# Kernel tuning notes

Measured on AMD Instinct MI355X. Metric: run time of the kernel, lower is better.

The kernel has to match this reference:

```python
import jax, jax.numpy as jnp
import numpy as np

B, L, H, F, D = 8, 2048, 1024, 256, 3  # batch, seq, d_model, adapter bottleneck, non-news domains
EPS = 1e-6  # annotated-transformer LayerNorm eps


def setup_inputs() -> dict:
    key = jax.random.key(0)
    ks = jax.random.split(key, 6)
    s1 = 1.0 / np.sqrt(H)
    s2 = 1.0 / np.sqrt(F)
    return {
        "x": jax.random.normal(ks[0], (B, L, H), jnp.float32),
        # per-domain LayerNorm params (SublayerConnection.norm)
        "ln_g": jnp.ones((D, H), jnp.float32),
        "ln_b": jnp.zeros((D, H), jnp.float32),
        # per-domain adapter FFN: Linear(H->F), ReLU, Linear(F->H)
        "W1": (jax.random.normal(ks[1], (D, F, H), jnp.float32) * s1),
        "b1": jnp.zeros((D, F), jnp.float32),
        "W2": (jax.random.normal(ks[2], (D, H, F), jnp.float32) * s2),
        "b2": jnp.zeros((D, H), jnp.float32),
        # per-domain gate Linear(2H -> 1), split into the x-half (gu) and adapter-half (gv)
        "gu": (jax.random.normal(ks[3], (D, H), jnp.float32) * s1),
        "gv": (jax.random.normal(ks[4], (D, H), jnp.float32) * s1),
        "gb": jnp.zeros((D,), jnp.float32),
    }


def reference(x, ln_g, ln_b, W1, b1, W2, b2, gu, gv, gb):
    # mix_output=True, used_domain_list=['news','book','bible','iwslt'],
    # target_domain='book' (in list -> no extra pass), dropout=eval (identity).
    mu = jnp.mean(x, axis=-1, keepdims=True)
    sd = jnp.std(x, axis=-1, keepdims=True, ddof=1)  # torch .std default (unbiased)
    xn = (x - mu) / (sd + EPS)                        # shared normalization stats
    # per-domain LayerNorm affine -> [D,B,L,H]
    h = xn[None] * ln_g[:, None, None, :] + ln_b[:, None, None, :]
    # adapter FFN (wo_residual_forward): Linear -> ReLU -> Linear
    mid = jax.nn.relu(jnp.einsum('dblh,dfh->dblf', h, W1) + b1[:, None, None, :])
    a = jnp.einsum('dblf,dhf->dblh', mid, W2) + b2[:, None, None, :]  # [D,B,L,H]
    # gate = sigmoid(Linear([x; a])) with W_gate split as [gu | gv]
    gate = jax.nn.sigmoid(
        jnp.einsum('blh,dh->dbl', x, gu)
        + jnp.einsum('dblh,dh->dbl', a, gv)
        + gb[:, None, None]
    )  # [D,B,L]
    # stacked sum includes 'news' contribution (= x), then outer residual +x:
    return 2.0 * x + jnp.sum(gate[..., None] * a, axis=0)
```

## Files before the change

### kernel.cpp

```cpp
#include <hip/hip_runtime.h>
#include <cstdint>

#define T_TOK 16384
#define H 1024
#define F 256
#define D 3
#define DF 768

typedef unsigned short u16;
typedef __attribute__((ext_vector_type(8))) short short8;
typedef __attribute__((ext_vector_type(4))) float floatx4;

__device__ __forceinline__ u16 f2bf(float f) {
  unsigned u = __float_as_uint(f);
  u += 0x7fff + ((u >> 16) & 1);
  return (u16)(u >> 16);
}
__device__ __forceinline__ float bf2f(u16 s) {
  return __uint_as_float(((unsigned)s) << 16);
}

__device__ __forceinline__ void gload_lds16(const void* g, void* l) {
  __builtin_amdgcn_global_load_lds(
      reinterpret_cast<const __attribute__((address_space(1))) void*>(
          reinterpret_cast<uintptr_t>(g)),
      reinterpret_cast<__attribute__((address_space(3))) void*>(
          reinterpret_cast<uintptr_t>(l)),
      16, 0, 0);
}

__device__ __forceinline__ float block_reduce_256(float v, float* red, int tid) {
  #pragma unroll
  for (int o = 32; o > 0; o >>= 1) v += __shfl_xor(v, o);
  __syncthreads();
  if ((tid & 63) == 0) red[tid >> 6] = v;
  __syncthreads();
  return red[0] + red[1] + red[2] + red[3];
}


__global__ __launch_bounds__(256)
void prep_elem(const float* __restrict__ W1, const float* __restrict__ lng,
               u16* __restrict__ W1p, const float* __restrict__ W2,
               u16* __restrict__ W2r)
{
  int idx = blockIdx.x * 256 + threadIdx.x;
  int stride = gridDim.x * 256;
  for (int i = idx; i < D * F * H; i += stride) {
    int h = i & (H - 1);
    int d = i / (F * H);
    W1p[i] = f2bf(W1[i] * lng[d * H + h]);
  }
  for (int i = idx; i < H * DF; i += stride) {
    int k = i % DF;
    int hh = i / DF;
    int d = k >> 8;
    int f = k & (F - 1);
    W2r[i] = f2bf(W2[((size_t)d * H + hh) * F + f]);
  }
}

__global__ __launch_bounds__(256)
void prep_dots(const float* __restrict__ W1, const float* __restrict__ lnb,
               const float* __restrict__ b1, const float* __restrict__ W2,
               const float* __restrict__ gv, const float* __restrict__ b2,
               const float* __restrict__ gb, float* __restrict__ b1p,
               float* __restrict__ wg, float* __restrict__ cg)
{
  __shared__ float red[4];
  int d = blockIdx.x >> 8;
  int f = blockIdx.x & 255;
  int tid = threadIdx.x;
  float s1 = 0.f, s2 = 0.f, s3 = 0.f;
  for (int h = tid; h < H; h += 256) {
    float w1v = W1[((size_t)d * F + f) * H + h];
    float gvv = gv[d * H + h];
    s1 += lnb[d * H + h] * w1v;
    s2 += W2[((size_t)d * H + h) * F + f] * gvv;
    if (f == 0) s3 += b2[d * H + h] * gvv;
  }
  float S1 = block_reduce_256(s1, red, tid);
  float S2 = block_reduce_256(s2, red, tid);
  if (tid == 0) {
    b1p[d * F + f] = b1[d * F + f] + S1;
    wg[d * F + f] = S2;
  }
  if (f == 0) {
    float S3 = block_reduce_256(s3, red, tid);
    if (tid == 0) cg[d] = gb[d] + S3;
  }
}

__global__ __launch_bounds__(256)
void ln_xu_kernel(const float* __restrict__ x, const float* __restrict__ gu,
                  u16* __restrict__ xn, float* __restrict__ xu)
{
  int t = blockIdx.x;
  int tid = threadIdx.x;
  const float4 xv = *reinterpret_cast<const float4*>(x + (size_t)t * H + tid * 4);
  const float4 g0 = *reinterpret_cast<const float4*>(gu + tid * 4);
  const float4 g1 = *reinterpret_cast<const float4*>(gu + H + tid * 4);
  const float4 g2 = *reinterpret_cast<const float4*>(gu + 2 * H + tid * 4);
  float s  = xv.x + xv.y + xv.z + xv.w;
  float sq = xv.x * xv.x + xv.y * xv.y + xv.z * xv.z + xv.w * xv.w;
  float d0 = xv.x * g0.x + xv.y * g0.y + xv.z * g0.z + xv.w * g0.w;
  float d1 = xv.x * g1.x + xv.y * g1.y + xv.z * g1.z + xv.w * g1.w;
  float d2 = xv.x * g2.x + xv.y * g2.y + xv.z * g2.z + xv.w * g2.w;
  #pragma unroll
  for (int o = 32; o > 0; o >>= 1) {
    s  += __shfl_xor(s, o);  sq += __shfl_xor(sq, o);
    d0 += __shfl_xor(d0, o); d1 += __shfl_xor(d1, o); d2 += __shfl_xor(d2, o);
  }
  __shared__ float red[4][5];
  int w = tid >> 6;
  if ((tid & 63) == 0) {
    red[w][0] = s; red[w][1] = sq; red[w][2] = d0; red[w][3] = d1; red[w][4] = d2;
  }
  __syncthreads();
  float S  = red[0][0] + red[1][0] + red[2][0] + red[3][0];
  float SQ = red[0][1] + red[1][1] + red[2][1] + red[3][1];
  float mu = S * (1.0f / H);
  float var = (SQ - (float)H * mu * mu) * (1.0f / (H - 1));
  float rs = 1.0f / (sqrtf(fmaxf(var, 0.0f)) + 1e-6f);
  ushort4 o4;
  o4.x = f2bf((xv.x - mu) * rs);
  o4.y = f2bf((xv.y - mu) * rs);
  o4.z = f2bf((xv.z - mu) * rs);
  o4.w = f2bf((xv.w - mu) * rs);
  *reinterpret_cast<ushort4*>(xn + (size_t)t * H + tid * 4) = o4;
  if (tid == 0) {
    xu[t]             = red[0][2] + red[1][2] + red[2][2] + red[3][2];
    xu[T_TOK + t]     = red[0][3] + red[1][3] + red[2][3] + red[3][3];
    xu[2 * T_TOK + t] = red[0][4] + red[1][4] + red[2][4] + red[3][4];
  }
}

template <int K, int NLD, int EPI>
__global__ __launch_bounds__(512, 4)
void gemm2p(const u16* __restrict__ A, const u16* __restrict__ Bm,
            const float* __restrict__ p0,
            const float* __restrict__ p1,
            const float* __restrict__ p2,
            const float* __restrict__ p3,
            u16* __restrict__ o16,
            float* __restrict__ o32,
            int nBy)
{
  constexpr int NT = K / 32;
  constexpr int BUF = 12288;
  extern __shared__ u16 LD[];

  const int tid = threadIdx.x, lane = tid & 63, w = tid >> 6;
  const int wm = w >> 2, wn = w & 3, lr = lane & 15, sl = lane >> 4;

  const int nwg = gridDim.x;
  const int wgs = (blockIdx.x & 7) * (nwg >> 3) + (blockIdx.x >> 3);
  const int by = wgs % nBy, bx = wgs / nBy;
  const int m0 = by * 128, n0 = bx * 256;

  const u16* Asrc = A + (size_t)m0 * K;
  const u16* Bsrc = Bm + (size_t)n0 * K;

  const int sc = (tid & 3) ^ ((tid >> 3) & 3);
  const int srcA  = (tid >> 2) * K + sc * 8;
  const int srcB1 = srcA + 128 * K;
  const int dstA  = w * 512;
  const int dstB0 = 4096 + w * 512;
  const int dstB1 = 8192 + w * 512;

  const int key = (lr >> 1) & 3;
  const int rsl = (sl ^ key) << 3;
  const int aoff = (wm * 64 + lr) * 32 + rsl;
  const int boff = 4096 + (wn * 64 + lr) * 32 + rsl;

  floatx4 acc[4][4] = {};
  short8 a[4], b[4];

#define STG(BP, T_) do { int kb_ = (T_) * 32; \
    gload_lds16(Asrc + srcA + kb_, (BP) + dstA); \
    gload_lds16(Bsrc + srcA + kb_, (BP) + dstB0); \
    gload_lds16(Bsrc + srcB1 + kb_, (BP) + dstB1); \
  } while (0)
#define LDAB(BP) do { \
    const u16* sa_ = (BP) + aoff; const u16* sb_ = (BP) + boff; \
    _Pragma("unroll") for (int i_ = 0; i_ < 4; ++i_) { \
      a[i_] = *reinterpret_cast<const short8*>(sa_ + i_ * 512); \
      b[i_] = *reinterpret_cast<const short8*>(sb_ + i_ * 512); } } while (0)
#define MMX() do { \
    _Pragma("unroll") for (int mf_ = 0; mf_ < 4; ++mf_) \
      _Pragma("unroll") for (int nf_ = 0; nf_ < 4; ++nf_) \
        acc[mf_][nf_] = __builtin_amdgcn_mfma_f32_16x16x32_bf16( \
            a[mf_], b[nf_], acc[mf_][nf_], 0, 0, 0); } while (0)

  STG(LD, 0);
  __syncthreads();

  #pragma unroll 1
  for (int t = 0; t < NT - 1; ++t) {
    u16* cur = LD + (t & 1) * BUF;
    u16* nxt = LD + ((t + 1) & 1) * BUF;
    STG(nxt, t + 1);
    LDAB(cur);
    MMX();
    __syncthreads();
  }
  LDAB(LD + ((NT - 1) & 1) * BUF);
  MMX();
  __syncthreads();

  if constexpr (EPI == 1) {
    float b1v[4], wgv[4];
    #pragma unroll
    for (int nf = 0; nf < 4; ++nf) {
      int col = n0 + wn * 64 + nf * 16 + lr;
      b1v[nf] = p0[col];
      wgv[nf] = p1[col];
    }
    float* red = (float*)LD;
    #pragma unroll
    for (int mf = 0; mf < 4; ++mf)
      #pragma unroll
      for (int i2 = 0; i2 < 4; ++i2) {
        float p = 0.f;
        #pragma unroll
        for (int nf = 0; nf < 4; ++nf)
          p += fmaxf(acc[mf][nf][i2] + b1v[nf], 0.f) * wgv[nf];
        p += __shfl_xor(p, 1); p += __shfl_xor(p, 2);
        p += __shfl_xor(p, 4); p += __shfl_xor(p, 8);
        if (lr == 0) red[wn * 128 + wm * 64 + mf * 16 + sl * 4 + i2] = p;
      }
    __syncthreads();
    const int d = bx;
    const float cgv = p3[d];
    #pragma unroll
    for (int mf = 0; mf < 4; ++mf)
      #pragma unroll
      for (int i2 = 0; i2 < 4; ++i2) {
        int rl = wm * 64 + mf * 16 + sl * 4 + i2;
        int r = m0 + rl;
        float logit = red[rl] + red[128 + rl] + red[256 + rl] + red[384 + rl]
                    + p2[(size_t)d * T_TOK + r] + cgv;
        float g = 1.f / (1.f + expf(-logit));
        #pragma unroll
        for (int nf = 0; nf < 4; ++nf) {
          int col = n0 + wn * 64 + nf * 16 + lr;
          float v = fmaxf(acc[mf][nf][i2] + b1v[nf], 0.f);
          o16[(size_t)r * NLD + col] = f2bf(v * g);
        }
        if (lr == 0 && wn == 0) o32[(size_t)d * T_TOK + r] = g;
      }
  } else {
    float b2v[3][4];
    #pragma unroll
    for (int dd = 0; dd < 3; ++dd)
      #pragma unroll
      for (int nf = 0; nf < 4; ++nf)
        b2v[dd][nf] = p2[dd * H + n0 + wn * 64 + nf * 16 + lr];
    #pragma unroll
    for (int mf = 0; mf < 4; ++mf)
      #pragma unroll
      for (int i2 = 0; i2 < 4; ++i2) {
        int r = m0 + wm * 64 + mf * 16 + sl * 4 + i2;
        float g0 = p1[r], g1 = p1[T_TOK + r], g2 = p1[2 * T_TOK + r];
        const float* xrow = p0 + (size_t)r * H;
        float* orow = o32 + (size_t)r * NLD;
        #pragma unroll
        for (int nf = 0; nf < 4; ++nf) {
          int col = n0 + wn * 64 + nf * 16 + lr;
          orow[col] = acc[mf][nf][i2] + 2.f * xrow[col]
                    + g0 * b2v[0][nf] + g1 * b2v[1][nf] + g2 * b2v[2][nf];
        }
      }
  }
#undef STG
#undef LDAB
#undef MMX
}


extern "C" void kernel_launch(void* const* d_in, const int* in_sizes, int n_in,
                              void* d_out, int out_size, void* d_ws, size_t ws_size,
                              hipStream_t stream) {
  const float* x   = (const float*)d_in[0];
  const float* lng = (const float*)d_in[1];
  const float* lnb = (const float*)d_in[2];
  const float* W1  = (const float*)d_in[3];
  const float* b1  = (const float*)d_in[4];
  const float* W2  = (const float*)d_in[5];
  const float* b2  = (const float*)d_in[6];
  const float* gu  = (const float*)d_in[7];
  const float* gv  = (const float*)d_in[8];
  const float* gb  = (const float*)d_in[9];
  float* out = (float*)d_out;

  char* ws = (char*)d_ws;
  u16* xn   = (u16*)ws;  ws += (size_t)T_TOK * H * 2;
  u16* mid  = (u16*)ws;  ws += (size_t)T_TOK * DF * 2;
  u16* W1p  = (u16*)ws;  ws += (size_t)DF * H * 2;
  u16* W2r  = (u16*)ws;  ws += (size_t)H * DF * 2;
  float* b1p  = (float*)ws;  ws += DF * 4;
  float* wg   = (float*)ws;  ws += DF * 4;
  float* cg   = (float*)ws;  ws += 256;
  float* xu   = (float*)ws;  ws += (size_t)D * T_TOK * 4;
  float* gate = (float*)ws;  ws += (size_t)D * T_TOK * 4;
  (void)ws_size; (void)in_sizes; (void)n_in; (void)out_size;

  hipFuncSetAttribute(reinterpret_cast<const void*>(&gemm2p<1024, DF, 1>),
                      hipFuncAttributeMaxDynamicSharedMemorySize, 49152);
  hipFuncSetAttribute(reinterpret_cast<const void*>(&gemm2p<768, H, 2>),
                      hipFuncAttributeMaxDynamicSharedMemorySize, 49152);

  prep_elem<<<3072, 256, 0, stream>>>(W1, lng, W1p, W2, W2r);
  prep_dots<<<DF, 256, 0, stream>>>(W1, lnb, b1, W2, gv, b2, gb, b1p, wg, cg);
  ln_xu_kernel<<<T_TOK, 256, 0, stream>>>(x, gu, xn, xu);
  gemm2p<1024, DF, 1><<<128 * 3, 512, 49152, stream>>>(
      xn, W1p, b1p, wg, xu, cg, mid, gate, 128);
  gemm2p<768, H, 2><<<128 * 4, 512, 49152, stream>>>(
      mid, W2r, x, gate, b2, nullptr, nullptr, out, 128);
}
```

Before: 132.6 us.

## Stage GEMM1 epilogue through LDS for coalesced stores and remap blocks per XCD

The first GEMM epilogue now writes the gated bf16 tile into padded LDS and then stores it to global memory as 16-byte vectors, replacing the scattered 2-byte per-lane stores. The workgroup-to-tile mapping changes so each XCD owns a contiguous range of 16 row-blocks and iterates over all column blocks (domains) of those rows. The goal is better L2 reuse of the A rows within an XCD. The cost is larger dynamic LDS (66KB) for GEMM1, which can lower occupancy, plus extra barriers.

```diff
diff --git a/kernel.cpp b/kernel.cpp
--- a/kernel.cpp
+++ b/kernel.cpp
@@ -144,7 +144,7 @@
             const float* __restrict__ p3,
             u16* __restrict__ o16,
             float* __restrict__ o32,
-            int nBy)
+            int nBx)
 {
   constexpr int NT = K / 32;
   constexpr int BUF = 12288;
@@ -153,9 +153,10 @@
   const int tid = threadIdx.x, lane = tid & 63, w = tid >> 6;
   const int wm = w >> 2, wn = w & 3, lr = lane & 15, sl = lane >> 4;
 
-  const int nwg = gridDim.x;
-  const int wgs = (blockIdx.x & 7) * (nwg >> 3) + (blockIdx.x >> 3);
-  const int by = wgs % nBy, bx = wgs / nBy;
+  const int bid = blockIdx.x;
+  const int xcd = bid & 7, idx = bid >> 3;
+  const int by = xcd * 16 + idx / nBx;
+  const int bx = idx % nBx;
   const int m0 = by * 128, n0 = bx * 256;
 
   const u16* Asrc = A + (size_t)m0 * K;
@@ -232,6 +233,7 @@
     __syncthreads();
     const int d = bx;
     const float cgv = p3[d];
+    float gv_[4][4];
     #pragma unroll
     for (int mf = 0; mf < 4; ++mf)
       #pragma unroll
@@ -241,14 +243,30 @@
         float logit = red[rl] + red[128 + rl] + red[256 + rl] + red[384 + rl]
                     + p2[(size_t)d * T_TOK + r] + cgv;
         float g = 1.f / (1.f + expf(-logit));
+        gv_[mf][i2] = g;
+        if (lr == 0 && wn == 0) o32[(size_t)d * T_TOK + r] = g;
+      }
+    __syncthreads();
+    #pragma unroll
+    for (int mf = 0; mf < 4; ++mf)
+      #pragma unroll
+      for (int i2 = 0; i2 < 4; ++i2) {
+        int rl = wm * 64 + mf * 16 + sl * 4 + i2;
         #pragma unroll
         for (int nf = 0; nf < 4; ++nf) {
-          int col = n0 + wn * 64 + nf * 16 + lr;
+          int cl = wn * 64 + nf * 16 + lr;
           float v = fmaxf(acc[mf][nf][i2] + b1v[nf], 0.f);
-          o16[(size_t)r * NLD + col] = f2bf(v * g);
+          LD[rl * 264 + cl] = f2bf(v * gv_[mf][i2]);
         }
-        if (lr == 0 && wn == 0) o32[(size_t)d * T_TOK + r] = g;
       }
+    __syncthreads();
+    #pragma unroll
+    for (int ps = 0; ps < 8; ++ps) {
+      int q = ps * 512 + tid;
+      int row = q >> 5, ch = q & 31;
+      short8 v = *reinterpret_cast<const short8*>(LD + row * 264 + ch * 8);
+      *reinterpret_cast<short8*>(&o16[(size_t)(m0 + row) * NLD + n0 + ch * 8]) = v;
+    }
   } else {
     float b2v[3][4];
     #pragma unroll
@@ -306,15 +324,15 @@
   (void)ws_size; (void)in_sizes; (void)n_in; (void)out_size;
 
   hipFuncSetAttribute(reinterpret_cast<const void*>(&gemm2p<1024, DF, 1>),
-                      hipFuncAttributeMaxDynamicSharedMemorySize, 49152);
+                      hipFuncAttributeMaxDynamicSharedMemorySize, 67584);
   hipFuncSetAttribute(reinterpret_cast<const void*>(&gemm2p<768, H, 2>),
                       hipFuncAttributeMaxDynamicSharedMemorySize, 49152);
 
   prep_elem<<<3072, 256, 0, stream>>>(W1, lng, W1p, W2, W2r);
   prep_dots<<<DF, 256, 0, stream>>>(W1, lnb, b1, W2, gv, b2, gb, b1p, wg, cg);
   ln_xu_kernel<<<T_TOK, 256, 0, stream>>>(x, gu, xn, xu);
-  gemm2p<1024, DF, 1><<<128 * 3, 512, 49152, stream>>>(
-      xn, W1p, b1p, wg, xu, cg, mid, gate, 128);
+  gemm2p<1024, DF, 1><<<128 * 3, 512, 67584, stream>>>(
+      xn, W1p, b1p, wg, xu, cg, mid, gate, 3);
   gemm2p<768, H, 2><<<128 * 4, 512, 49152, stream>>>(
-      mid, W2r, x, gate, b2, nullptr, nullptr, out, 128);
-}
+      mid, W2r, x, gate, b2, nullptr, nullptr, out, 4);
+}
```

After: 127.3 us. -4.1%, faster.

## Shrink GEMM tiles to 128x128, single-buffer K=64 stages, split gate into own kernel

Applied to the files above, without the earlier changes.

The two-GEMM pipeline now uses 256-thread workgroups with 128x128 tiles and 64-wide K steps in a single LDS buffer, replacing the 512-thread, 128x256, double-buffered version. Grid mapping is reorganized per XCD so each one covers contiguous row blocks. The gating logit and sigmoid scaling move out of the first GEMM's epilogue into a separate per-token gate_kernel that rereads and rewrites the mid buffer. The first GEMM's epilogue now stages its tile through LDS for coalesced stores. The goal is better occupancy and a simpler epilogue, at the cost of no load/compute overlap, an extra kernel launch, and an extra pass over mid.

```diff
diff --git a/kernel.cpp b/kernel.cpp
--- a/kernel.cpp
+++ b/kernel.cpp
@@ -135,120 +135,120 @@
   }
 }
 
+__global__ __launch_bounds__(192)
+void gate_kernel(u16* __restrict__ mid, const float* __restrict__ wg,
+                 const float* __restrict__ xu, const float* __restrict__ cg,
+                 float* __restrict__ gateOut)
+{
+  int t = blockIdx.x;
+  int tid = threadIdx.x;
+  int w = tid >> 6;
+  int lane = tid & 63;
+  size_t base = (size_t)t * DF + tid * 4;
+  ushort4 mv = *reinterpret_cast<const ushort4*>(mid + base);
+  float4 wv = *reinterpret_cast<const float4*>(wg + tid * 4);
+  float m0 = bf2f(mv.x), m1 = bf2f(mv.y), m2 = bf2f(mv.z), m3 = bf2f(mv.w);
+  float dot = m0 * wv.x + m1 * wv.y + m2 * wv.z + m3 * wv.w;
+  #pragma unroll
+  for (int o = 32; o > 0; o >>= 1) dot += __shfl_xor(dot, o);
+  float logit = xu[(size_t)w * T_TOK + t] + dot + cg[w];
+  float g = 1.0f / (1.0f + expf(-logit));
+  mv.x = f2bf(m0 * g); mv.y = f2bf(m1 * g);
+  mv.z = f2bf(m2 * g); mv.w = f2bf(m3 * g);
+  *reinterpret_cast<ushort4*>(mid + base) = mv;
+  if (lane == 0) gateOut[(size_t)w * T_TOK + t] = g;
+}
+
 template <int K, int NLD, int EPI>
-__global__ __launch_bounds__(512, 4)
-void gemm2p(const u16* __restrict__ A, const u16* __restrict__ Bm,
+__global__ __launch_bounds__(256, 3)
+void gemm97(const u16* __restrict__ A, const u16* __restrict__ Bm,
             const float* __restrict__ p0,
             const float* __restrict__ p1,
             const float* __restrict__ p2,
-            const float* __restrict__ p3,
             u16* __restrict__ o16,
             float* __restrict__ o32,
-            int nBy)
-{
-  constexpr int NT = K / 32;
-  constexpr int BUF = 12288;
+            int nBx, int byX)
+{
+  constexpr int NT = K / 64;
   extern __shared__ u16 LD[];
 
   const int tid = threadIdx.x, lane = tid & 63, w = tid >> 6;
-  const int wm = w >> 2, wn = w & 3, lr = lane & 15, sl = lane >> 4;
-
-  const int nwg = gridDim.x;
-  const int wgs = (blockIdx.x & 7) * (nwg >> 3) + (blockIdx.x >> 3);
-  const int by = wgs % nBy, bx = wgs / nBy;
-  const int m0 = by * 128, n0 = bx * 256;
+  const int wm = w >> 1, wn = w & 1, lr = lane & 15, sl = lane >> 4;
+
+  const int bid = blockIdx.x;
+  const int xcd = bid & 7, idx = bid >> 3;
+  const int by = xcd * byX + idx / nBx;
+  const int bx = idx % nBx;
+  const int m0 = by * 128, n0 = bx * 128;
 
   const u16* Asrc = A + (size_t)m0 * K;
   const u16* Bsrc = Bm + (size_t)n0 * K;
 
-  const int sc = (tid & 3) ^ ((tid >> 3) & 3);
-  const int srcA  = (tid >> 2) * K + sc * 8;
-  const int srcB1 = srcA + 128 * K;
-  const int dstA  = w * 512;
-  const int dstB0 = 4096 + w * 512;
-  const int dstB1 = 8192 + w * 512;
-
-  const int key = (lr >> 1) & 3;
-  const int rsl = (sl ^ key) << 3;
-  const int aoff = (wm * 64 + lr) * 32 + rsl;
-  const int boff = 4096 + (wn * 64 + lr) * 32 + rsl;
+  const int sc8 = ((tid & 7) ^ ((tid >> 3) & 7)) << 3;
+  const int grow = tid >> 3;
+  const int w512 = w * 512;
+
+  const int rk = lr & 7;
+  const int arow = (wm * 64 + lr) * 64;
+  const int brow = 8192 + (wn * 64 + lr) * 64;
 
   floatx4 acc[4][4] = {};
   short8 a[4], b[4];
 
-#define STG(BP, T_) do { int kb_ = (T_) * 32; \
-    gload_lds16(Asrc + srcA + kb_, (BP) + dstA); \
-    gload_lds16(Bsrc + srcA + kb_, (BP) + dstB0); \
-    gload_lds16(Bsrc + srcB1 + kb_, (BP) + dstB1); \
+#define STG(kb_) do { \
+    _Pragma("unroll") for (int it_ = 0; it_ < 4; ++it_) \
+      gload_lds16(Asrc + (size_t)(it_ * 32 + grow) * K + sc8 + (kb_), \
+                  LD + it_ * 2048 + w512); \
+    _Pragma("unroll") for (int it_ = 0; it_ < 4; ++it_) \
+      gload_lds16(Bsrc + (size_t)(it_ * 32 + grow) * K + sc8 + (kb_), \
+                  LD + 8192 + it_ * 2048 + w512); \
   } while (0)
-#define LDAB(BP) do { \
-    const u16* sa_ = (BP) + aoff; const u16* sb_ = (BP) + boff; \
+#define LDAB(ks) do { \
+    const int ch_ = (((ks) * 4 + sl) ^ rk) << 3; \
     _Pragma("unroll") for (int i_ = 0; i_ < 4; ++i_) { \
-      a[i_] = *reinterpret_cast<const short8*>(sa_ + i_ * 512); \
-      b[i_] = *reinterpret_cast<const short8*>(sb_ + i_ * 512); } } while (0)
+      a[i_] = *reinterpret_cast<const short8*>(LD + arow + i_ * 1024 + ch_); \
+      b[i_] = *reinterpret_cast<const short8*>(LD + brow + i_ * 1024 + ch_); } \
+  } while (0)
 #define MMX() do { \
     _Pragma("unroll") for (int mf_ = 0; mf_ < 4; ++mf_) \
       _Pragma("unroll") for (int nf_ = 0; nf_ < 4; ++nf_) \
         acc[mf_][nf_] = __builtin_amdgcn_mfma_f32_16x16x32_bf16( \
             a[mf_], b[nf_], acc[mf_][nf_], 0, 0, 0); } while (0)
 
-  STG(LD, 0);
-  __syncthreads();
-
   #pragma unroll 1
-  for (int t = 0; t < NT - 1; ++t) {
-    u16* cur = LD + (t & 1) * BUF;
-    u16* nxt = LD + ((t + 1) & 1) * BUF;
-    STG(nxt, t + 1);
-    LDAB(cur);
-    MMX();
+  for (int t = 0; t < NT; ++t) {
+    STG(t * 64);
     __syncthreads();
-  }
-  LDAB(LD + ((NT - 1) & 1) * BUF);
-  MMX();
-  __syncthreads();
+    LDAB(0); MMX();
+    LDAB(1); MMX();
+    __syncthreads();
+  }
 
   if constexpr (EPI == 1) {
-    float b1v[4], wgv[4];
-    #pragma unroll
-    for (int nf = 0; nf < 4; ++nf) {
-      int col = n0 + wn * 64 + nf * 16 + lr;
-      b1v[nf] = p0[col];
-      wgv[nf] = p1[col];
-    }
-    float* red = (float*)LD;
-    #pragma unroll
-    for (int mf = 0; mf < 4; ++mf)
-      #pragma unroll
-      for (int i2 = 0; i2 < 4; ++i2) {
-        float p = 0.f;
-        #pragma unroll
-        for (int nf = 0; nf < 4; ++nf)
-          p += fmaxf(acc[mf][nf][i2] + b1v[nf], 0.f) * wgv[nf];
-        p += __shfl_xor(p, 1); p += __shfl_xor(p, 2);
-        p += __shfl_xor(p, 4); p += __shfl_xor(p, 8);
-        if (lr == 0) red[wn * 128 + wm * 64 + mf * 16 + sl * 4 + i2] = p;
-      }
-    __syncthreads();
-    const int d = bx;
-    const float cgv = p3[d];
+    float b1v[4];
+    #pragma unroll
+    for (int nf = 0; nf < 4; ++nf)
+      b1v[nf] = p0[n0 + wn * 64 + nf * 16 + lr];
     #pragma unroll
     for (int mf = 0; mf < 4; ++mf)
       #pragma unroll
       for (int i2 = 0; i2 < 4; ++i2) {
         int rl = wm * 64 + mf * 16 + sl * 4 + i2;
-        int r = m0 + rl;
-        float logit = red[rl] + red[128 + rl] + red[256 + rl] + red[384 + rl]
-                    + p2[(size_t)d * T_TOK + r] + cgv;
-        float g = 1.f / (1.f + expf(-logit));
         #pragma unroll
         for (int nf = 0; nf < 4; ++nf) {
-          int col = n0 + wn * 64 + nf * 16 + lr;
-          float v = fmaxf(acc[mf][nf][i2] + b1v[nf], 0.f);
-          o16[(size_t)r * NLD + col] = f2bf(v * g);
+          int cl = wn * 64 + nf * 16 + lr;
+          LD[rl * 136 + cl] = f2bf(fmaxf(acc[mf][nf][i2] + b1v[nf], 0.f));
         }
-        if (lr == 0 && wn == 0) o32[(size_t)d * T_TOK + r] = g;
       }
+    __syncthreads();
+    #pragma unroll
+    for (int it = 0; it < 8; ++it) {
+      int q = it * 256 + tid;
+      int row = q >> 4, ch = q & 15;
+      short8 v = *reinterpret_cast<const short8*>(LD + row * 136 + ch * 8);
+      *reinterpret_cast<short8*>(
+          &o16[(size_t)(m0 + row) * NLD + n0 + ch * 8]) = v;
+    }
   } else {
     float b2v[3][4];
     #pragma unroll
@@ -305,16 +305,17 @@
   float* gate = (float*)ws;  ws += (size_t)D * T_TOK * 4;
   (void)ws_size; (void)in_sizes; (void)n_in; (void)out_size;
 
-  hipFuncSetAttribute(reinterpret_cast<const void*>(&gemm2p<1024, DF, 1>),
-                      hipFuncAttributeMaxDynamicSharedMemorySize, 49152);
-  hipFuncSetAttribute(reinterpret_cast<const void*>(&gemm2p<768, H, 2>),
-                      hipFuncAttributeMaxDynamicSharedMemorySize, 49152);
+  hipFuncSetAttribute(reinterpret_cast<const void*>(&gemm97<1024, DF, 1>),
+                      hipFuncAttributeMaxDynamicSharedMemorySize, 34816);
+  hipFuncSetAttribute(reinterpret_cast<const void*>(&gemm97<768, H, 2>),
+                      hipFuncAttributeMaxDynamicSharedMemorySize, 32768);
 
   prep_elem<<<3072, 256, 0, stream>>>(W1, lng, W1p, W2, W2r);
   prep_dots<<<DF, 256, 0, stream>>>(W1, lnb, b1, W2, gv, b2, gb, b1p, wg, cg);
   ln_xu_kernel<<<T_TOK, 256, 0, stream>>>(x, gu, xn, xu);
-  gemm2p<1024, DF, 1><<<128 * 3, 512, 49152, stream>>>(
-      xn, W1p, b1p, wg, xu, cg, mid, gate, 128);
-  gemm2p<768, H, 2><<<128 * 4, 512, 49152, stream>>>(
-      mid, W2r, x, gate, b2, nullptr, nullptr, out, 128);
-}
+  gemm97<1024, DF, 1><<<128 * 6, 256, 34816, stream>>>(
+      xn, W1p, b1p, nullptr, nullptr, mid, nullptr, 6, 16);
+  gate_kernel<<<T_TOK, 192, 0, stream>>>(mid, wg, xu, cg, gate);
+  gemm97<768, H, 2><<<128 * 8, 256, 32768, stream>>>(
+      mid, W2r, x, gate, b2, nullptr, out, 8, 16);
+}
```

Result: faster. 126.2 us (-4.9%).
